# Kernel optimization log

Hardware: AMD Instinct MI355X
Metric: run time of the kernel (lower is better)

Reference implementation:

```python
import jax, jax.numpy as jnp
import numpy as np

N, C_IN, F = 64, 1024, 20          # batch, backbone channels, grid size (640/32)
N_CLASSES = 80
A = 3                               # anchors in this layer (mask [6,7,8])
STRIDE = 32
C = N_CLASSES + 5                   # 85
C_OUT = A * C                       # 255
ANCHORS = np.array([[116.0, 90.0], [156.0, 198.0], [373.0, 326.0]], np.float32) / STRIDE


def setup_inputs() -> dict:
    key = jax.random.key(0)
    k1, k2 = jax.random.split(key)
    xin = jax.random.normal(k1, (N, C_IN, F, F), jnp.float32)
    conv_w = jax.random.normal(k2, (C_OUT, C_IN, 1, 1), jnp.float32) * 0.02
    conv_b = jnp.zeros((C_OUT,), jnp.float32)
    return {"xin": xin, "conv_w": conv_w, "conv_b": conv_b}


def reference(xin, conv_w, conv_b):
    anchors = jnp.asarray(ANCHORS, dtype=xin.dtype)  # [A, 2], grid units
    # 1x1 conv head: [N, C_OUT, F, F]
    out = jax.lax.conv_general_dilated(xin, conv_w, window_strides=(1, 1),
                                       padding="VALID")
    out = out + conv_b[None, :, None, None]
    # [N, A, C, F, F] -> [N, A, F(y), F(x), C]
    out = out.reshape(N, A, C, F, F).transpose(0, 1, 3, 4, 2)

    xy = jax.nn.sigmoid(out[..., :2])       # sigmoid on tx, ty
    wh = out[..., 2:4]                      # raw tw, th
    objcls = jax.nn.sigmoid(out[..., 4:])   # sigmoid on obj + classes

    grid = jnp.arange(F, dtype=xin.dtype)
    px = xy[..., 0] + grid[None, None, None, :]   # + x_shift (varies along last spatial dim)
    py = xy[..., 1] + grid[None, None, :, None]   # + y_shift
    pw = jnp.exp(wh[..., 0]) * anchors[:, 0].reshape(1, A, 1, 1)
    ph = jnp.exp(wh[..., 1]) * anchors[:, 1].reshape(1, A, 1, 1)

    boxes = jnp.stack([px, py, pw, ph], axis=-1) * STRIDE  # back to pixel coords
    pred = jnp.concatenate([boxes, objcls], axis=-1)       # [N, A, F, F, C]
    return pred.reshape(N, -1, C)                           # [N, A*F*F, C]
```

## Files before the change

### kernel.cpp

```cpp
#include <hip/hip_runtime.h>
#include <hip/hip_bf16.h>
#include <math.h>

#define CIN    1024
#define S_TOT  400
#define COUT   255
#define NCH    85
#define NIMG   64
#define BN     80
#define BK     64
#define NSTEP  16
#define NTHR   256

#define XS_BASE   16384
#define LDS_BYTES (16384 + 10240)
#define WSTEP_B   32768

typedef __attribute__((ext_vector_type(8))) short bf16x8;
typedef __attribute__((ext_vector_type(4))) float f32x4;

struct __attribute__((aligned(4))) f4u { float x, y, z, w; };

__device__ __forceinline__ int wOff(int co, int kg) {
    return (co << 7) + ((kg << 4) ^ ((co & 7) << 4));
}
__device__ __forceinline__ int xOff(int s, int kg) {
    return XS_BASE + (s << 7) + ((kg << 4) ^ (((s >> 1) & 7) << 4));
}

__device__ __forceinline__ unsigned pk2(float a, float b) {
    __hip_bfloat162 h;
    h.x = __float2bfloat16(a);
    h.y = __float2bfloat16(b);
    return *reinterpret_cast<unsigned*>(&h);
}

__device__ __forceinline__ float sigmoidf_(float v) {
    return 1.0f / (1.0f + expf(-v));
}

__device__ __forceinline__ void gload_lds16(const void* g, void* l) {
    __builtin_amdgcn_global_load_lds(
        (const __attribute__((address_space(1))) unsigned int*)g,
        (__attribute__((address_space(3))) unsigned int*)l,
        16, 0, 0);
}

__global__ __launch_bounds__(256) void w_pre(const float* __restrict__ w,
                                             unsigned short* __restrict__ wbf) {
    int g = blockIdx.x * 256 + threadIdx.x;
    int co    = g >> 7;
    int kgAll = g & 127;
    int k     = kgAll << 3;
    int step  = k >> 6;
    int kg    = (k >> 3) & 7;
    union { unsigned short u[8]; bf16x8 v; } pk;
    if (co < COUT) {
        const float* src = w + co * CIN + k;
        #pragma unroll
        for (int j = 0; j < 8; ++j) {
            __hip_bfloat16 h = __float2bfloat16(src[j]);
            pk.u[j] = *reinterpret_cast<unsigned short*>(&h);
        }
    } else {
        #pragma unroll
        for (int j = 0; j < 8; ++j) pk.u[j] = 0;
    }
    char* dst = reinterpret_cast<char*>(wbf) + step * WSTEP_B + wOff(co, kg);
    *reinterpret_cast<bf16x8*>(dst) = pk.v;
}

__device__ __forceinline__ void stageX(const float* base, char* smem, int s0, int kg) {
    float2 cu[8];
    #pragma unroll
    for (int j = 0; j < 8; ++j) cu[j] = *(const float2*)(base + j * S_TOT);
    union { unsigned u[4]; bf16x8 v; } r0, r1;
    #pragma unroll
    for (int j = 0; j < 4; ++j) {
        r0.u[j] = pk2(cu[2 * j].x, cu[2 * j + 1].x);
        r1.u[j] = pk2(cu[2 * j].y, cu[2 * j + 1].y);
    }
    *(bf16x8*)(smem + xOff(s0,     kg)) = r0.v;
    *(bf16x8*)(smem + xOff(s0 + 1, kg)) = r1.v;
}

__global__ __launch_bounds__(NTHR, 4) void yolo_mfma(
    const float* __restrict__ xin,
    const unsigned short* __restrict__ wbf,
    const float* __restrict__ bias,
    float* __restrict__ out)
{
    __shared__ __align__(16) char smem[LDS_BYTES];

    const int n     = blockIdx.z;
    const int cob   = blockIdx.y * 128;
    const int sbase = blockIdx.x * BN;
    const int tid   = threadIdx.x;
    const int lane  = tid & 63;
    const int wid   = tid >> 6;

    const float* xin_n = xin + (size_t)n * (CIN * S_TOT);

    const int kg0 = tid / 40;
    const int sp0 = tid % 40;
    const int kg1 = (256 + tid) / 40;
    const int sp1 = (256 + tid) % 40;
    const bool dual = tid < 64;

    f32x4 acc[2][5] = {};

    const int co_w = wid * 32;
    const int llo  = lane & 15;
    const int lhi  = lane >> 4;

    for (int t = 0; t < NSTEP; ++t) {
        const char* wg = (const char*)wbf + (size_t)t * WSTEP_B + (size_t)cob * 128;
        #pragma unroll
        for (int i = 0; i < 4; ++i)
            gload_lds16(wg + i * 4096 + (size_t)tid * 16,
                        smem + i * 4096 + wid * 1024);

        const float* xt = xin_n + (size_t)t * (BK * S_TOT) + sbase;
        stageX(xt + kg0 * 8 * S_TOT + 2 * sp0, smem, 2 * sp0, kg0);
        if (dual)
            stageX(xt + kg1 * 8 * S_TOT + 2 * sp1, smem, 2 * sp1, kg1);

        __syncthreads();

        #pragma unroll
        for (int ks = 0; ks < 2; ++ks) {
            const int kgr = ks * 4 + lhi;
            bf16x8 a0 = *(bf16x8*)(smem + wOff(co_w + llo,      kgr));
            bf16x8 a1 = *(bf16x8*)(smem + wOff(co_w + 16 + llo, kgr));
            #pragma unroll
            for (int ni = 0; ni < 5; ++ni) {
                bf16x8 b = *(bf16x8*)(smem + xOff(ni * 16 + llo, kgr));
                acc[0][ni] = __builtin_amdgcn_mfma_f32_16x16x32_bf16(a0, b, acc[0][ni], 0, 0, 0);
                acc[1][ni] = __builtin_amdgcn_mfma_f32_16x16x32_bf16(a1, b, acc[1][ni], 0, 0, 0);
            }
        }
        __syncthreads();
    }

    const float anchW[3] = {116.0f, 156.0f, 373.0f};
    const float anchH[3] = {90.0f, 198.0f, 326.0f};

    #pragma unroll
    for (int mi = 0; mi < 2; ++mi) {
        const int co0 = cob + co_w + mi * 16 + lhi * 4;
        const int aW  = co0 / NCH;
        const int c0  = co0 - aW * NCH;
        const bool whole = (c0 <= NCH - 4) && (co0 + 3 < COUT);
        float bv[4];
        #pragma unroll
        for (int r = 0; r < 4; ++r)
            bv[r] = (co0 + r < COUT) ? bias[co0 + r] : 0.0f;

        #pragma unroll
        for (int ni = 0; ni < 5; ++ni) {
            const int s  = sbase + ni * 16 + llo;
            const float sx = (float)(s % 20);
            const float sy = (float)(s / 20);
            if (whole) {
                float r4[4];
                #pragma unroll
                for (int r = 0; r < 4; ++r) {
                    const int c = c0 + r;
                    const float v = acc[mi][ni][r] + bv[r];
                    float res;
                    if (c == 0)      res = (sigmoidf_(v) + sx) * 32.0f;
                    else if (c == 1) res = (sigmoidf_(v) + sy) * 32.0f;
                    else if (c == 2) res = expf(v) * anchW[aW];
                    else if (c == 3) res = expf(v) * anchH[aW];
                    else             res = sigmoidf_(v);
                    r4[r] = res;
                }
                f4u* p = (f4u*)(out + (size_t)n * 102000 + aW * 34000 + s * 85 + c0);
                f4u val = {r4[0], r4[1], r4[2], r4[3]};
                *p = val;
            } else {
                #pragma unroll
                for (int r = 0; r < 4; ++r) {
                    const int co = co0 + r;
                    if (co < COUT) {
                        const int a2 = co / NCH;
                        const int c  = co - a2 * NCH;
                        const float v = acc[mi][ni][r] + bv[r];
                        float res;
                        if (c == 0)      res = (sigmoidf_(v) + sx) * 32.0f;
                        else if (c == 1) res = (sigmoidf_(v) + sy) * 32.0f;
                        else if (c == 2) res = expf(v) * anchW[a2];
                        else if (c == 3) res = expf(v) * anchH[a2];
                        else             res = sigmoidf_(v);
                        out[(size_t)n * 102000 + a2 * 34000 + s * 85 + c] = res;
                    }
                }
            }
        }
    }
}

extern "C" void kernel_launch(void* const* d_in, const int* in_sizes, int n_in,
                              void* d_out, int out_size, void* d_ws, size_t ws_size,
                              hipStream_t stream) {
    const float* xin  = (const float*)d_in[0];
    const float* w    = (const float*)d_in[1];
    const float* bias = (const float*)d_in[2];
    float* out = (float*)d_out;
    unsigned short* wbf = (unsigned short*)d_ws;

    w_pre<<<128, 256, 0, stream>>>(w, wbf);
    yolo_mfma<<<dim3(S_TOT / BN, 2, NIMG), NTHR, 0, stream>>>(xin, wbf, bias, out);
}
```

Measured before the change: 68.94 us.

## Retile conv head: all channels per block, weights read directly from global

Each block now covers all 256 output channels for 16 spatial positions of two images, instead of 128 channels by 80 positions of one image. The bf16 weights are repacked to a [k-group][co] layout and read straight from global/L2 into registers for each MFMA, so they no longer go through LDS. Only the input activations are staged in LDS, in two halves of 512 input channels, which cuts the barrier count from 32 to 3. The aim is to stop recomputing the X tile per channel half and to reduce synchronisation, at the cost of more L2 traffic for weights and smaller spatial tiles.

Result: slower. 70.58 us (+2.4%).

```diff
diff --git a/kernel.cpp b/kernel.cpp
--- a/kernel.cpp
+++ b/kernel.cpp
@@ -7,25 +7,19 @@
 #define COUT   255
 #define NCH    85
 #define NIMG   64
-#define BN     80
-#define BK     64
-#define NSTEP  16
+#define SB     16
+#define NI     2
 #define NTHR   256
 
-#define XS_BASE   16384
-#define LDS_BYTES (16384 + 10240)
-#define WSTEP_B   32768
+#define LDS_BYTES 32768
 
 typedef __attribute__((ext_vector_type(8))) short bf16x8;
 typedef __attribute__((ext_vector_type(4))) float f32x4;
 
 struct __attribute__((aligned(4))) f4u { float x, y, z, w; };
 
-__device__ __forceinline__ int wOff(int co, int kg) {
-    return (co << 7) + ((kg << 4) ^ ((co & 7) << 4));
-}
-__device__ __forceinline__ int xOff(int s, int kg) {
-    return XS_BASE + (s << 7) + ((kg << 4) ^ (((s >> 1) & 7) << 4));
+__device__ __forceinline__ int xOff2(int img, int s, int gl) {
+    return img * 16384 + (s << 10) + ((gl << 4) ^ (((s >> 1) & 7) << 4));
 }
 
 __device__ __forceinline__ unsigned pk2(float a, float b) {
@@ -39,24 +33,14 @@
     return 1.0f / (1.0f + expf(-v));
 }
 
-__device__ __forceinline__ void gload_lds16(const void* g, void* l) {
-    __builtin_amdgcn_global_load_lds(
-        (const __attribute__((address_space(1))) unsigned int*)g,
-        (__attribute__((address_space(3))) unsigned int*)l,
-        16, 0, 0);
-}
-
-__global__ __launch_bounds__(256) void w_pre(const float* __restrict__ w,
-                                             unsigned short* __restrict__ wbf) {
-    int g = blockIdx.x * 256 + threadIdx.x;
-    int co    = g >> 7;
-    int kgAll = g & 127;
-    int k     = kgAll << 3;
-    int step  = k >> 6;
-    int kg    = (k >> 3) & 7;
+__global__ __launch_bounds__(256) void w_pre2(const float* __restrict__ w,
+                                              unsigned short* __restrict__ wbf) {
+    int gidx = blockIdx.x * 256 + threadIdx.x;
+    int co = gidx & 255;
+    int g  = gidx >> 8;
     union { unsigned short u[8]; bf16x8 v; } pk;
     if (co < COUT) {
-        const float* src = w + co * CIN + k;
+        const float* src = w + (size_t)co * CIN + g * 8;
         #pragma unroll
         for (int j = 0; j < 8; ++j) {
             __hip_bfloat16 h = __float2bfloat16(src[j]);
@@ -66,25 +50,10 @@
         #pragma unroll
         for (int j = 0; j < 8; ++j) pk.u[j] = 0;
     }
-    char* dst = reinterpret_cast<char*>(wbf) + step * WSTEP_B + wOff(co, kg);
-    *reinterpret_cast<bf16x8*>(dst) = pk.v;
+    *reinterpret_cast<bf16x8*>((char*)wbf + ((size_t)(g << 8) + co) * 16) = pk.v;
 }
 
-__device__ __forceinline__ void stageX(const float* base, char* smem, int s0, int kg) {
-    float2 cu[8];
-    #pragma unroll
-    for (int j = 0; j < 8; ++j) cu[j] = *(const float2*)(base + j * S_TOT);
-    union { unsigned u[4]; bf16x8 v; } r0, r1;
-    #pragma unroll
-    for (int j = 0; j < 4; ++j) {
-        r0.u[j] = pk2(cu[2 * j].x, cu[2 * j + 1].x);
-        r1.u[j] = pk2(cu[2 * j].y, cu[2 * j + 1].y);
-    }
-    *(bf16x8*)(smem + xOff(s0,     kg)) = r0.v;
-    *(bf16x8*)(smem + xOff(s0 + 1, kg)) = r1.v;
-}
-
-__global__ __launch_bounds__(NTHR, 4) void yolo_mfma(
+__global__ __launch_bounds__(NTHR, 4) void yolo_mfma2(
     const float* __restrict__ xin,
     const unsigned short* __restrict__ wbf,
     const float* __restrict__ bias,
@@ -92,62 +61,69 @@
 {
     __shared__ __align__(16) char smem[LDS_BYTES];
 
-    const int n     = blockIdx.z;
-    const int cob   = blockIdx.y * 128;
-    const int sbase = blockIdx.x * BN;
-    const int tid   = threadIdx.x;
-    const int lane  = tid & 63;
-    const int wid   = tid >> 6;
-
-    const float* xin_n = xin + (size_t)n * (CIN * S_TOT);
-
-    const int kg0 = tid / 40;
-    const int sp0 = tid % 40;
-    const int kg1 = (256 + tid) / 40;
-    const int sp1 = (256 + tid) % 40;
-    const bool dual = tid < 64;
-
-    f32x4 acc[2][5] = {};
-
-    const int co_w = wid * 32;
+    const int sb  = blockIdx.x * SB;
+    const int n0  = blockIdx.y * NI;
+    const int tid = threadIdx.x;
+    const int lane = tid & 63;
+    const int wid  = tid >> 6;
     const int llo  = lane & 15;
     const int lhi  = lane >> 4;
 
-    for (int t = 0; t < NSTEP; ++t) {
-        const char* wg = (const char*)wbf + (size_t)t * WSTEP_B + (size_t)cob * 128;
+    f32x4 acc[4][NI] = {};
+
+    for (int h = 0; h < 2; ++h) {
+        if (h) __syncthreads();
+
         #pragma unroll
-        for (int i = 0; i < 4; ++i)
-            gload_lds16(wg + i * 4096 + (size_t)tid * 16,
-                        smem + i * 4096 + wid * 1024);
-
-        const float* xt = xin_n + (size_t)t * (BK * S_TOT) + sbase;
-        stageX(xt + kg0 * 8 * S_TOT + 2 * sp0, smem, 2 * sp0, kg0);
-        if (dual)
-            stageX(xt + kg1 * 8 * S_TOT + 2 * sp1, smem, 2 * sp1, kg1);
-
+        for (int p = 0; p < 4; ++p) {
+            int unit = p * 256 + tid;
+            int img  = unit >> 9;
+            int gl   = (unit >> 3) & 63;
+            int sp   = unit & 7;
+            const float* src = xin
+                + ((size_t)(n0 + img) * CIN + h * 512 + gl * 8) * S_TOT
+                + sb + 2 * sp;
+            float2 cu[8];
+            #pragma unroll
+            for (int j = 0; j < 8; ++j) cu[j] = *(const float2*)(src + j * S_TOT);
+            union { unsigned u[4]; bf16x8 v; } r0, r1;
+            #pragma unroll
+            for (int j = 0; j < 4; ++j) {
+                r0.u[j] = pk2(cu[2 * j].x, cu[2 * j + 1].x);
+                r1.u[j] = pk2(cu[2 * j].y, cu[2 * j + 1].y);
+            }
+            *(bf16x8*)(smem + xOff2(img, 2 * sp,     gl)) = r0.v;
+            *(bf16x8*)(smem + xOff2(img, 2 * sp + 1, gl)) = r1.v;
+        }
         __syncthreads();
 
-        #pragma unroll
-        for (int ks = 0; ks < 2; ++ks) {
-            const int kgr = ks * 4 + lhi;
-            bf16x8 a0 = *(bf16x8*)(smem + wOff(co_w + llo,      kgr));
-            bf16x8 a1 = *(bf16x8*)(smem + wOff(co_w + 16 + llo, kgr));
+        #pragma unroll 4
+        for (int kk = 0; kk < 16; ++kk) {
+            const int gA = (h * 16 + kk) * 4 + lhi;
+            const int gl = kk * 4 + lhi;
+            bf16x8 b[NI];
             #pragma unroll
-            for (int ni = 0; ni < 5; ++ni) {
-                bf16x8 b = *(bf16x8*)(smem + xOff(ni * 16 + llo, kgr));
-                acc[0][ni] = __builtin_amdgcn_mfma_f32_16x16x32_bf16(a0, b, acc[0][ni], 0, 0, 0);
-                acc[1][ni] = __builtin_amdgcn_mfma_f32_16x16x32_bf16(a1, b, acc[1][ni], 0, 0, 0);
+            for (int im = 0; im < NI; ++im)
+                b[im] = *(bf16x8*)(smem + xOff2(im, llo, gl));
+            #pragma unroll
+            for (int mi = 0; mi < 4; ++mi) {
+                const int co = wid * 64 + mi * 16 + llo;
+                bf16x8 a = *(const bf16x8*)((const char*)wbf
+                                            + ((size_t)(gA << 8) + co) * 16);
+                #pragma unroll
+                for (int im = 0; im < NI; ++im)
+                    acc[mi][im] = __builtin_amdgcn_mfma_f32_16x16x32_bf16(
+                        a, b[im], acc[mi][im], 0, 0, 0);
             }
         }
-        __syncthreads();
     }
 
     const float anchW[3] = {116.0f, 156.0f, 373.0f};
     const float anchH[3] = {90.0f, 198.0f, 326.0f};
 
     #pragma unroll
-    for (int mi = 0; mi < 2; ++mi) {
-        const int co0 = cob + co_w + mi * 16 + lhi * 4;
+    for (int mi = 0; mi < 4; ++mi) {
+        const int co0 = wid * 64 + mi * 16 + lhi * 4;
         const int aW  = co0 / NCH;
         const int c0  = co0 - aW * NCH;
         const bool whole = (c0 <= NCH - 4) && (co0 + 3 < COUT);
@@ -157,8 +133,9 @@
             bv[r] = (co0 + r < COUT) ? bias[co0 + r] : 0.0f;
 
         #pragma unroll
-        for (int ni = 0; ni < 5; ++ni) {
-            const int s  = sbase + ni * 16 + llo;
+        for (int im = 0; im < NI; ++im) {
+            const int n = n0 + im;
+            const int s = sb + llo;
             const float sx = (float)(s % 20);
             const float sy = (float)(s / 20);
             if (whole) {
@@ -166,7 +143,7 @@
                 #pragma unroll
                 for (int r = 0; r < 4; ++r) {
                     const int c = c0 + r;
-                    const float v = acc[mi][ni][r] + bv[r];
+                    const float v = acc[mi][im][r] + bv[r];
                     float res;
                     if (c == 0)      res = (sigmoidf_(v) + sx) * 32.0f;
                     else if (c == 1) res = (sigmoidf_(v) + sy) * 32.0f;
@@ -185,7 +162,7 @@
                     if (co < COUT) {
                         const int a2 = co / NCH;
                         const int c  = co - a2 * NCH;
-                        const float v = acc[mi][ni][r] + bv[r];
+                        const float v = acc[mi][im][r] + bv[r];
                         float res;
                         if (c == 0)      res = (sigmoidf_(v) + sx) * 32.0f;
                         else if (c == 1) res = (sigmoidf_(v) + sy) * 32.0f;
@@ -209,6 +186,6 @@
     float* out = (float*)d_out;
     unsigned short* wbf = (unsigned short*)d_ws;
 
-    w_pre<<<128, 256, 0, stream>>>(w, wbf);
-    yolo_mfma<<<dim3(S_TOT / BN, 2, NIMG), NTHR, 0, stream>>>(xin, wbf, bias, out);
+    w_pre2<<<128, 256, 0, stream>>>(w, wbf);
+    yolo_mfma2<<<dim3(S_TOT / SB, NIMG / NI), NTHR, 0, stream>>>(xin, wbf, bias, out);
 }
```

## Flatten batch-spatial into one N dimension with full-COUT 256x128 tiles

Applied to the files above, without the earlier changes.

Treats batch and spatial positions as a single flattened dimension and gives each 512-thread block all 256 output channels against 128 flat positions. X is then read once rather than once per half of the channel range, and each wave computes a 64x64 tile that reuses its A and B fragments across 16 MFMAs. X staging switches to float4 loads. The costs are a larger LDS footprint, more accumulator registers, occupancy lowered to 2 blocks per CU, and a per-element div/mod to recover image and position in the epilogue.

Result: slower. 72.92 us (+5.8%).

```diff
diff --git a/kernel.cpp b/kernel.cpp
--- a/kernel.cpp
+++ b/kernel.cpp
@@ -7,13 +7,14 @@
 #define COUT   255
 #define NCH    85
 #define NIMG   64
-#define BN     80
+#define NFLAT  (NIMG * S_TOT)
+#define BN     128
 #define BK     64
 #define NSTEP  16
-#define NTHR   256
-
-#define XS_BASE   16384
-#define LDS_BYTES (16384 + 10240)
+#define NTHR   512
+
+#define BB        32768
+#define LDS_BYTES 49152
 #define WSTEP_B   32768
 
 typedef __attribute__((ext_vector_type(8))) short bf16x8;
@@ -24,8 +25,8 @@
 __device__ __forceinline__ int wOff(int co, int kg) {
     return (co << 7) + ((kg << 4) ^ ((co & 7) << 4));
 }
-__device__ __forceinline__ int xOff(int s, int kg) {
-    return XS_BASE + (s << 7) + ((kg << 4) ^ (((s >> 1) & 7) << 4));
+__device__ __forceinline__ int xBoff(int s, int kg) {
+    return BB + (s << 7) + ((kg << 4) ^ (((s >> 1) & 7) << 4));
 }
 
 __device__ __forceinline__ unsigned pk2(float a, float b) {
@@ -56,7 +57,7 @@
     int kg    = (k >> 3) & 7;
     union { unsigned short u[8]; bf16x8 v; } pk;
     if (co < COUT) {
-        const float* src = w + co * CIN + k;
+        const float* src = w + (size_t)co * CIN + k;
         #pragma unroll
         for (int j = 0; j < 8; ++j) {
             __hip_bfloat16 h = __float2bfloat16(src[j]);
@@ -70,21 +71,7 @@
     *reinterpret_cast<bf16x8*>(dst) = pk.v;
 }
 
-__device__ __forceinline__ void stageX(const float* base, char* smem, int s0, int kg) {
-    float2 cu[8];
-    #pragma unroll
-    for (int j = 0; j < 8; ++j) cu[j] = *(const float2*)(base + j * S_TOT);
-    union { unsigned u[4]; bf16x8 v; } r0, r1;
-    #pragma unroll
-    for (int j = 0; j < 4; ++j) {
-        r0.u[j] = pk2(cu[2 * j].x, cu[2 * j + 1].x);
-        r1.u[j] = pk2(cu[2 * j].y, cu[2 * j + 1].y);
-    }
-    *(bf16x8*)(smem + xOff(s0,     kg)) = r0.v;
-    *(bf16x8*)(smem + xOff(s0 + 1, kg)) = r1.v;
-}
-
-__global__ __launch_bounds__(NTHR, 4) void yolo_mfma(
+__global__ __launch_bounds__(NTHR, 2) void yolo_m97(
     const float* __restrict__ xin,
     const unsigned short* __restrict__ wbf,
     const float* __restrict__ bias,
@@ -92,52 +79,63 @@
 {
     __shared__ __align__(16) char smem[LDS_BYTES];
 
-    const int n     = blockIdx.z;
-    const int cob   = blockIdx.y * 128;
-    const int sbase = blockIdx.x * BN;
-    const int tid   = threadIdx.x;
-    const int lane  = tid & 63;
-    const int wid   = tid >> 6;
-
-    const float* xin_n = xin + (size_t)n * (CIN * S_TOT);
-
-    const int kg0 = tid / 40;
-    const int sp0 = tid % 40;
-    const int kg1 = (256 + tid) / 40;
-    const int sp1 = (256 + tid) % 40;
-    const bool dual = tid < 64;
-
-    f32x4 acc[2][5] = {};
-
-    const int co_w = wid * 32;
+    const int tile = blockIdx.x * BN;
+    const int tid  = threadIdx.x;
+    const int lane = tid & 63;
+    const int w8   = tid >> 6;
     const int llo  = lane & 15;
     const int lhi  = lane >> 4;
+    const int co_w = (w8 >> 1) * 64;
+    const int s_w  = (w8 & 1) * 64;
+
+    const int bllo = tid & 31;
+    const int bgrp = tid >> 5;
+    const int flatB = tile + 4 * bllo;
+    const int nB = flatB / S_TOT;
+    const int sB = flatB - nB * S_TOT;
+    const float* xsrcB = xin + ((size_t)nB * CIN + bgrp * 8) * S_TOT + sB;
+
+    f32x4 acc[4][4] = {};
 
     for (int t = 0; t < NSTEP; ++t) {
-        const char* wg = (const char*)wbf + (size_t)t * WSTEP_B + (size_t)cob * 128;
+        const char* wg = (const char*)wbf + (size_t)t * WSTEP_B;
         #pragma unroll
         for (int i = 0; i < 4; ++i)
-            gload_lds16(wg + i * 4096 + (size_t)tid * 16,
-                        smem + i * 4096 + wid * 1024);
-
-        const float* xt = xin_n + (size_t)t * (BK * S_TOT) + sbase;
-        stageX(xt + kg0 * 8 * S_TOT + 2 * sp0, smem, 2 * sp0, kg0);
-        if (dual)
-            stageX(xt + kg1 * 8 * S_TOT + 2 * sp1, smem, 2 * sp1, kg1);
-
+            gload_lds16(wg + i * 8192 + (size_t)tid * 16,
+                        smem + i * 8192 + w8 * 1024);
+
+        if (tid < 256) {
+            const float* src = xsrcB + (size_t)t * (BK * S_TOT);
+            union F4 { float4 v; float f[4]; } cu[8];
+            #pragma unroll
+            for (int j = 0; j < 8; ++j) cu[j].v = *(const float4*)(src + j * S_TOT);
+            #pragma unroll
+            for (int r = 0; r < 4; ++r) {
+                union { unsigned u4[4]; bf16x8 b; } rr;
+                #pragma unroll
+                for (int jj = 0; jj < 4; ++jj)
+                    rr.u4[jj] = pk2(cu[2 * jj].f[r], cu[2 * jj + 1].f[r]);
+                *(bf16x8*)(smem + xBoff(4 * bllo + r, bgrp)) = rr.b;
+            }
+        }
         __syncthreads();
 
         #pragma unroll
         for (int ks = 0; ks < 2; ++ks) {
             const int kgr = ks * 4 + lhi;
-            bf16x8 a0 = *(bf16x8*)(smem + wOff(co_w + llo,      kgr));
-            bf16x8 a1 = *(bf16x8*)(smem + wOff(co_w + 16 + llo, kgr));
-            #pragma unroll
-            for (int ni = 0; ni < 5; ++ni) {
-                bf16x8 b = *(bf16x8*)(smem + xOff(ni * 16 + llo, kgr));
-                acc[0][ni] = __builtin_amdgcn_mfma_f32_16x16x32_bf16(a0, b, acc[0][ni], 0, 0, 0);
-                acc[1][ni] = __builtin_amdgcn_mfma_f32_16x16x32_bf16(a1, b, acc[1][ni], 0, 0, 0);
-            }
+            bf16x8 afr[4], bfr[4];
+            #pragma unroll
+            for (int mi = 0; mi < 4; ++mi)
+                afr[mi] = *(bf16x8*)(smem + wOff(co_w + mi * 16 + llo, kgr));
+            #pragma unroll
+            for (int ns = 0; ns < 4; ++ns)
+                bfr[ns] = *(bf16x8*)(smem + xBoff(s_w + ns * 16 + llo, kgr));
+            #pragma unroll
+            for (int mi = 0; mi < 4; ++mi)
+                #pragma unroll
+                for (int ns = 0; ns < 4; ++ns)
+                    acc[mi][ns] = __builtin_amdgcn_mfma_f32_16x16x32_bf16(
+                        afr[mi], bfr[ns], acc[mi][ns], 0, 0, 0);
         }
         __syncthreads();
     }
@@ -146,8 +144,8 @@
     const float anchH[3] = {90.0f, 198.0f, 326.0f};
 
     #pragma unroll
-    for (int mi = 0; mi < 2; ++mi) {
-        const int co0 = cob + co_w + mi * 16 + lhi * 4;
+    for (int mi = 0; mi < 4; ++mi) {
+        const int co0 = co_w + mi * 16 + lhi * 4;
         const int aW  = co0 / NCH;
         const int c0  = co0 - aW * NCH;
         const bool whole = (c0 <= NCH - 4) && (co0 + 3 < COUT);
@@ -157,8 +155,10 @@
             bv[r] = (co0 + r < COUT) ? bias[co0 + r] : 0.0f;
 
         #pragma unroll
-        for (int ni = 0; ni < 5; ++ni) {
-            const int s  = sbase + ni * 16 + llo;
+        for (int ns = 0; ns < 4; ++ns) {
+            const int flat = tile + s_w + ns * 16 + llo;
+            const int n = flat / S_TOT;
+            const int s = flat - n * S_TOT;
             const float sx = (float)(s % 20);
             const float sy = (float)(s / 20);
             if (whole) {
@@ -166,7 +166,7 @@
                 #pragma unroll
                 for (int r = 0; r < 4; ++r) {
                     const int c = c0 + r;
-                    const float v = acc[mi][ni][r] + bv[r];
+                    const float v = acc[mi][ns][r] + bv[r];
                     float res;
                     if (c == 0)      res = (sigmoidf_(v) + sx) * 32.0f;
                     else if (c == 1) res = (sigmoidf_(v) + sy) * 32.0f;
@@ -175,9 +175,9 @@
                     else             res = sigmoidf_(v);
                     r4[r] = res;
                 }
-                f4u* p = (f4u*)(out + (size_t)n * 102000 + aW * 34000 + s * 85 + c0);
+                f4u* pp = (f4u*)(out + (size_t)n * 102000 + aW * 34000 + s * 85 + c0);
                 f4u val = {r4[0], r4[1], r4[2], r4[3]};
-                *p = val;
+                *pp = val;
             } else {
                 #pragma unroll
                 for (int r = 0; r < 4; ++r) {
@@ -185,7 +185,7 @@
                     if (co < COUT) {
                         const int a2 = co / NCH;
                         const int c  = co - a2 * NCH;
-                        const float v = acc[mi][ni][r] + bv[r];
+                        const float v = acc[mi][ns][r] + bv[r];
                         float res;
                         if (c == 0)      res = (sigmoidf_(v) + sx) * 32.0f;
                         else if (c == 1) res = (sigmoidf_(v) + sy) * 32.0f;
@@ -210,5 +210,5 @@
     unsigned short* wbf = (unsigned short*)d_ws;
 
     w_pre<<<128, 256, 0, stream>>>(w, wbf);
-    yolo_mfma<<<dim3(S_TOT / BN, 2, NIMG), NTHR, 0, stream>>>(xin, wbf, bias, out);
-}
+    yolo_m97<<<NFLAT / BN, NTHR, 0, stream>>>(xin, wbf, bias, out);
+}
```
